# Kernel tuning notes

Measured on AMD Instinct MI355X. Metric: run time of the kernel, lower is better.

Reference implementation:

```python
import jax, jax.numpy as jnp
import numpy as np

NUM_HEADS = 16
EMBED_DIM = 1024
HEAD_DIM = EMBED_DIM // NUM_HEADS  # 64


def setup_inputs() -> dict:
    key = jax.random.key(0)
    k1, k2, k3 = jax.random.split(key, 3)
    x = jax.random.normal(k1, (2, 2048, EMBED_DIM), dtype=jnp.float32)
    # torch Linear(head_dim, 3*head_dim): weight [3*hd, hd], bias [3*hd]
    # stored here as W_qkv [hd, 3*hd] so that y = x @ W_qkv + b
    lim = 1.0 / np.sqrt(HEAD_DIM)
    W_qkv = jax.random.uniform(k2, (HEAD_DIM, 3 * HEAD_DIM), minval=-lim, maxval=lim, dtype=jnp.float32)
    b_qkv = jax.random.uniform(k3, (3 * HEAD_DIM,), minval=-lim, maxval=lim, dtype=jnp.float32)
    return {"x": x, "W_qkv": W_qkv, "b_qkv": b_qkv}


def reference(x, W_qkv, b_qkv):
    B, T, E = x.shape
    # [B, T, E] -> [B, H, T, hd]
    xh = x.reshape(B, T, NUM_HEADS, HEAD_DIM).transpose(0, 2, 1, 3)
    qkv = xh @ W_qkv + b_qkv  # [B, H, T, 3*hd], shared weights across heads
    q, k, v = jnp.split(qkv, 3, axis=-1)
    scale = 1.0 / jnp.sqrt(jnp.asarray(HEAD_DIM, dtype=x.dtype))
    scores = jnp.einsum('bhqd,bhkd->bhqk', q, k) * scale  # [B, H, T, T]
    attn = jax.nn.softmax(scores, axis=-1)
    out = jnp.einsum('bhqk,bhkd->bhqd', attn, v)  # [B, H, T, hd]
    return out.transpose(0, 2, 1, 3).reshape(B, T, E)
```

## Files before the change

### kernel.cpp

```cpp
#include <hip/hip_runtime.h>
#include <hip/hip_bf16.h>

#define T_SEQ   2048
#define EMBED   1024
#define HD      64
#define NHEADS  16
#define NBH     32
#define QSCALE  0.18033688011112042f

typedef __attribute__((ext_vector_type(8))) short short8;
typedef __attribute__((ext_vector_type(4))) float f32x4;
typedef __attribute__((ext_vector_type(2))) unsigned int uint2v;

#if __has_builtin(__builtin_amdgcn_exp2f)
#define EXP2F __builtin_amdgcn_exp2f
#else
#define EXP2F exp2f
#endif

__device__ __forceinline__ ushort bf16r(float f) {
  union { float f; unsigned u; } v; v.f = f;
  return (ushort)((v.u + 0x8000u) >> 16);
}

__device__ __forceinline__ unsigned pk2bf_perm(float a, float b) {
  union { float f; unsigned u; } ua, ub; ua.f = a; ub.f = b;
  return __builtin_amdgcn_perm(ub.u + 0x8000u, ua.u + 0x8000u, 0x07060302u);
}
#if __has_builtin(__builtin_amdgcn_cvt_pk_bf16_f32)
typedef __attribute__((ext_vector_type(2))) __bf16 bf16x2;
__device__ __forceinline__ unsigned pkbf(float a, float b) {
  union { bf16x2 v; unsigned u; } c;
  c.v = __builtin_amdgcn_cvt_pk_bf16_f32(a, b);
  return c.u;
}
#else
#define pkbf pk2bf_perm
#endif

__device__ __forceinline__ void async16(const ushort* g, ushort* l) {
  __builtin_amdgcn_global_load_lds(
      (const __attribute__((address_space(1))) unsigned int*)g,
      (__attribute__((address_space(3))) unsigned int*)l, 16, 0, 0);
}

__global__ __launch_bounds__(256) void prep_w(const float* __restrict__ W,
                                              ushort* __restrict__ Wg) {
  const int i = blockIdx.x * 256 + threadIdx.x;
  const int d = i / 192, c = i - d * 192;
  const int phys = c * 64 + (((d >> 3) ^ (c & 7)) << 3) + (d & 7);
  Wg[phys] = bf16r(W[i]);
}

__global__ __launch_bounds__(256) void qkv_proj(
    const float* __restrict__ x, const ushort* __restrict__ Wg,
    const float* __restrict__ bias,
    ushort* __restrict__ Qws, ushort* __restrict__ Kws,
    ushort* __restrict__ Vtws) {
  __shared__ ushort WtL[192 * 64];
  __shared__ float bl[192];

  const int bx = blockIdx.x;
  const int b  = bx >> 9;
  const int h  = (bx >> 5) & 15;
  const int t0 = (bx & 31) * 64;
  const int tid = threadIdx.x;
  const int wave = tid >> 6, lane = tid & 63;
  const int quad = lane >> 4, n16 = lane & 15;

  const int trow = t0 + wave * 16 + n16;
  const float* xr = x + ((size_t)(b * T_SEQ + trow)) * EMBED + h * HD;
  short8 xa[2];
#pragma unroll
  for (int ks = 0; ks < 2; ks++) {
    f32x4 v0 = *(const f32x4*)(xr + ks * 32 + quad * 8);
    f32x4 v1 = *(const f32x4*)(xr + ks * 32 + quad * 8 + 4);
    short8 f;
    ((unsigned*)&f)[0] = pkbf(v0[0], v0[1]);
    ((unsigned*)&f)[1] = pkbf(v0[2], v0[3]);
    ((unsigned*)&f)[2] = pkbf(v1[0], v1[1]);
    ((unsigned*)&f)[3] = pkbf(v1[2], v1[3]);
    xa[ks] = f;
  }

#pragma unroll
  for (int it = 0; it < 6; it++)
    async16(Wg + it * 2048 + tid * 8, WtL + it * 2048 + wave * 512);
  if (tid < 192) bl[tid] = bias[tid];
  __syncthreads();

  const int bh = b * NHEADS + h;
  const size_t qkbase = (size_t)bh * T_SEQ * HD;
  const int tw = t0 + wave * 16;
  const int sw = n16 & 7;

#pragma unroll
  for (int nt = 0; nt < 12; nt++) {
    const ushort* wrow = WtL + (nt * 16 + n16) * 64;
    const short8 wb0 = *(short8*)(wrow + ((quad ^ sw) << 3));
    const short8 wb1 = *(short8*)(wrow + (((4 | quad) ^ sw) << 3));
    const float bv = bl[nt * 16 + n16];
    f32x4 acc = (f32x4){0.f, 0.f, 0.f, 0.f};
    acc = __builtin_amdgcn_mfma_f32_16x16x32_bf16(xa[0], wb0, acc, 0, 0, 0);
    acc = __builtin_amdgcn_mfma_f32_16x16x32_bf16(xa[1], wb1, acc, 0, 0, 0);
    if (nt < 4) {
      const int d = nt * 16 + n16;
#pragma unroll
      for (int r = 0; r < 4; r++)
        Qws[qkbase + (size_t)(tw + quad * 4 + r) * HD + d] =
            bf16r((acc[r] + bv) * QSCALE);
    } else if (nt < 8) {
      const int d = (nt - 4) * 16 + n16;
#pragma unroll
      for (int r = 0; r < 4; r++)
        Kws[qkbase + (size_t)(tw + quad * 4 + r) * HD + d] =
            bf16r(acc[r] + bv);
    } else {
      const int d = (nt - 8) * 16 + n16;
      const int tcol = tw + quad * 4;
      uint2v pk;
      pk.x = pkbf(acc[0] + bv, acc[1] + bv);
      pk.y = pkbf(acc[2] + bv, acc[3] + bv);
      *(uint2v*)(Vtws + (size_t)(bh * HD + d) * T_SEQ + tcol) = pk;
    }
  }
}

__global__ __launch_bounds__(256) void flash_attn(
    const ushort* __restrict__ Qws, const ushort* __restrict__ Kws,
    const ushort* __restrict__ Vtws, float* __restrict__ out) {
  __shared__ ushort Ks[2][64 * 64];
  __shared__ ushort Vs[2][64 * 64];
  __shared__ ushort Ps[4 * 16 * 64];

  const int bx = blockIdx.x;
  const int bh = bx & 31;
  const int q0 = (bx >> 5) * 64;
  const int b = bh >> 4, h = bh & 15;
  const int tid = threadIdx.x;
  const int wave = tid >> 6, lane = tid & 63;
  const int quad = lane >> 4, n16 = lane & 15;

  const ushort* Qb = Qws + (size_t)bh * T_SEQ * HD;
  const ushort* Kb = Kws + (size_t)bh * T_SEQ * HD;
  const ushort* Vb = Vtws + (size_t)bh * HD * T_SEQ;

  short8 qa[2];
#pragma unroll
  for (int ks = 0; ks < 2; ks++) {
    const int row = q0 + wave * 16 + n16;
    qa[ks] = *(const short8*)(Qb + (size_t)row * HD + ks * 32 + quad * 8);
  }

  const int sr = tid >> 3, sp = tid & 7;
  const int sl = (sp ^ (sr & 7)) * 8;
  const ushort* srcK0 = Kb + (size_t)sr * HD + sl;
  const ushort* srcK1 = Kb + (size_t)(sr + 32) * HD + sl;
  const ushort* srcV0 = Vb + (size_t)sr * T_SEQ + sl;
  const ushort* srcV1 = Vb + (size_t)(sr + 32) * T_SEQ + sl;

  int foff[2];
#pragma unroll
  for (int ks = 0; ks < 2; ks++)
    foff[ks] = n16 * 64 + ((((ks << 2) | quad) ^ (n16 & 7)) << 3);

  f32x4 o[4];
  float lsum = 0.f;
#pragma unroll
  for (int nt = 0; nt < 4; nt++) o[nt] = (f32x4){0.f, 0.f, 0.f, 0.f};

  ushort* Pw = Ps + wave * 1024;

  async16(srcK0, Ks[0] + wave * 512);
  async16(srcK1, Ks[0] + 2048 + wave * 512);
  async16(srcV0, Vs[0] + wave * 512);
  async16(srcV1, Vs[0] + 2048 + wave * 512);
  __syncthreads();

  for (int kt = 0; kt < 32; kt++) {
    const int bsel = kt & 1;
    if (kt < 31) {
      const size_t kK = (size_t)(kt + 1) * 64 * HD;
      const size_t kV = (size_t)(kt + 1) * 64;
      async16(srcK0 + kK, Ks[bsel ^ 1] + wave * 512);
      async16(srcK1 + kK, Ks[bsel ^ 1] + 2048 + wave * 512);
      async16(srcV0 + kV, Vs[bsel ^ 1] + wave * 512);
      async16(srcV1 + kV, Vs[bsel ^ 1] + 2048 + wave * 512);
    }
    const ushort* Kt = Ks[bsel];
    const ushort* Vt = Vs[bsel];

    f32x4 s[4];
#pragma unroll
    for (int nt = 0; nt < 4; nt++) {
      const short8 ka0 = *(short8*)(Kt + (nt << 10) + foff[0]);
      const short8 ka1 = *(short8*)(Kt + (nt << 10) + foff[1]);
      f32x4 acc = (f32x4){0.f, 0.f, 0.f, 0.f};
      acc = __builtin_amdgcn_mfma_f32_16x16x32_bf16(ka0, qa[0], acc, 0, 0, 0);
      acc = __builtin_amdgcn_mfma_f32_16x16x32_bf16(ka1, qa[1], acc, 0, 0, 0);
      s[nt] = acc;
    }

#pragma unroll
    for (int nt = 0; nt < 4; nt++) {
      float p0 = EXP2F(s[nt][0]), p1 = EXP2F(s[nt][1]);
      float p2 = EXP2F(s[nt][2]), p3 = EXP2F(s[nt][3]);
      lsum += (p0 + p1) + (p2 + p3);
      uint2v pk;
      pk.x = pkbf(p0, p1);
      pk.y = pkbf(p2, p3);
      *(uint2v*)(Pw + n16 * 64 +
                 ((((nt << 1) | (quad >> 1)) ^ (n16 & 7)) << 3) +
                 ((quad & 1) << 2)) = pk;
    }

    short8 pa0 = *(short8*)(Pw + foff[0]);
    short8 pa1 = *(short8*)(Pw + foff[1]);
#pragma unroll
    for (int nt = 0; nt < 4; nt++) {
      const short8 vb0 = *(short8*)(Vt + (nt << 10) + foff[0]);
      const short8 vb1 = *(short8*)(Vt + (nt << 10) + foff[1]);
      o[nt] = __builtin_amdgcn_mfma_f32_16x16x32_bf16(pa0, vb0, o[nt], 0, 0, 0);
      o[nt] = __builtin_amdgcn_mfma_f32_16x16x32_bf16(pa1, vb1, o[nt], 0, 0, 0);
    }
    __syncthreads();
  }

  lsum += __shfl_xor(lsum, 16, 64);
  lsum += __shfl_xor(lsum, 32, 64);
  float* Lw = (float*)Pw;
  if (lane < 16) Lw[n16] = lsum;

#pragma unroll
  for (int r = 0; r < 4; r++) {
    const int row = q0 + wave * 16 + quad * 4 + r;
    const float rl = 1.0f / Lw[quad * 4 + r];
#pragma unroll
    for (int nt = 0; nt < 4; nt++) {
      const int d = nt * 16 + n16;
      out[(size_t)(b * T_SEQ + row) * EMBED + h * HD + d] = o[nt][r] * rl;
    }
  }
}

extern "C" void kernel_launch(void* const* d_in, const int* in_sizes, int n_in,
                              void* d_out, int out_size, void* d_ws, size_t ws_size,
                              hipStream_t stream) {
  (void)in_sizes; (void)n_in; (void)out_size; (void)ws_size;
  const float* x    = (const float*)d_in[0];
  const float* W    = (const float*)d_in[1];
  const float* bias = (const float*)d_in[2];
  float* out = (float*)d_out;

  const size_t elems = (size_t)NBH * T_SEQ * HD;
  ushort* Qws  = (ushort*)d_ws;
  ushort* Kws  = Qws + elems;
  ushort* Vtws = Kws + elems;
  ushort* Wg   = Vtws + elems;

  prep_w<<<dim3(48), dim3(256), 0, stream>>>(W, Wg);
  qkv_proj<<<dim3(1024), dim3(256), 0, stream>>>(x, Wg, bias, Qws, Kws, Vtws);
  flash_attn<<<dim3(1024), dim3(256), 0, stream>>>(Qws, Kws, Vtws, out);
}
```

Baseline: 135.9 us.

## Double query rows per wave and move P transpose into registers via permlane swaps

Each block now handles 128 query rows instead of 64, with each wave computing two 16-row halves. Every K/V tile loaded into LDS therefore feeds twice as many MFMAs, and the grid shrinks to 512 blocks. The P matrix is no longer written to and re-read from shared memory. It is rearranged into the MFMA A-operand layout with permlane32/permlane16 swap instructions, and the final row sums are broadcast by shuffle. The cost is more registers per thread and fewer blocks, which may lower occupancy and leave some CUs with less work.

```diff
diff --git a/kernel.cpp b/kernel.cpp
--- a/kernel.cpp
+++ b/kernel.cpp
@@ -11,6 +11,7 @@
 typedef __attribute__((ext_vector_type(8))) short short8;
 typedef __attribute__((ext_vector_type(4))) float f32x4;
 typedef __attribute__((ext_vector_type(2))) unsigned int uint2v;
+typedef __attribute__((ext_vector_type(4))) unsigned int uint4v;
 
 #if __has_builtin(__builtin_amdgcn_exp2f)
 #define EXP2F __builtin_amdgcn_exp2f
@@ -37,6 +38,23 @@
 #else
 #define pkbf pk2bf_perm
 #endif
+
+__device__ __forceinline__ uint2v pl32swap(unsigned a, unsigned b) {
+#if __has_builtin(__builtin_amdgcn_permlane32_swap)
+  return __builtin_amdgcn_permlane32_swap(a, b, false, false);
+#else
+  asm("v_permlane32_swap_b32 %0, %1" : "+v"(a), "+v"(b));
+  return (uint2v){a, b};
+#endif
+}
+__device__ __forceinline__ uint2v pl16swap(unsigned a, unsigned b) {
+#if __has_builtin(__builtin_amdgcn_permlane16_swap)
+  return __builtin_amdgcn_permlane16_swap(a, b, false, false);
+#else
+  asm("v_permlane16_swap_b32 %0, %1" : "+v"(a), "+v"(b));
+  return (uint2v){a, b};
+#endif
+}
 
 __device__ __forceinline__ void async16(const ushort* g, ushort* l) {
   __builtin_amdgcn_global_load_lds(
@@ -131,11 +149,10 @@
     const ushort* __restrict__ Vtws, float* __restrict__ out) {
   __shared__ ushort Ks[2][64 * 64];
   __shared__ ushort Vs[2][64 * 64];
-  __shared__ ushort Ps[4 * 16 * 64];
 
   const int bx = blockIdx.x;
   const int bh = bx & 31;
-  const int q0 = (bx >> 5) * 64;
+  const int q0 = (bx >> 5) * 128;
   const int b = bh >> 4, h = bh & 15;
   const int tid = threadIdx.x;
   const int wave = tid >> 6, lane = tid & 63;
@@ -145,12 +162,14 @@
   const ushort* Kb = Kws + (size_t)bh * T_SEQ * HD;
   const ushort* Vb = Vtws + (size_t)bh * HD * T_SEQ;
 
-  short8 qa[2];
-#pragma unroll
-  for (int ks = 0; ks < 2; ks++) {
-    const int row = q0 + wave * 16 + n16;
-    qa[ks] = *(const short8*)(Qb + (size_t)row * HD + ks * 32 + quad * 8);
-  }
+  short8 qa[2][2];
+#pragma unroll
+  for (int hf = 0; hf < 2; hf++)
+#pragma unroll
+    for (int ks = 0; ks < 2; ks++) {
+      const int row = q0 + wave * 32 + hf * 16 + n16;
+      qa[hf][ks] = *(const short8*)(Qb + (size_t)row * HD + ks * 32 + quad * 8);
+    }
 
   const int sr = tid >> 3, sp = tid & 7;
   const int sl = (sp ^ (sr & 7)) * 8;
@@ -164,12 +183,12 @@
   for (int ks = 0; ks < 2; ks++)
     foff[ks] = n16 * 64 + ((((ks << 2) | quad) ^ (n16 & 7)) << 3);
 
-  f32x4 o[4];
-  float lsum = 0.f;
-#pragma unroll
-  for (int nt = 0; nt < 4; nt++) o[nt] = (f32x4){0.f, 0.f, 0.f, 0.f};
-
-  ushort* Pw = Ps + wave * 1024;
+  f32x4 o[2][4];
+  float ls[2] = {0.f, 0.f};
+#pragma unroll
+  for (int hf = 0; hf < 2; hf++)
+#pragma unroll
+    for (int nt = 0; nt < 4; nt++) o[hf][nt] = (f32x4){0.f, 0.f, 0.f, 0.f};
 
   async16(srcK0, Ks[0] + wave * 512);
   async16(srcK1, Ks[0] + 2048 + wave * 512);
@@ -190,55 +209,77 @@
     const ushort* Kt = Ks[bsel];
     const ushort* Vt = Vs[bsel];
 
-    f32x4 s[4];
+    f32x4 s0[4], s1[4];
 #pragma unroll
     for (int nt = 0; nt < 4; nt++) {
       const short8 ka0 = *(short8*)(Kt + (nt << 10) + foff[0]);
       const short8 ka1 = *(short8*)(Kt + (nt << 10) + foff[1]);
-      f32x4 acc = (f32x4){0.f, 0.f, 0.f, 0.f};
-      acc = __builtin_amdgcn_mfma_f32_16x16x32_bf16(ka0, qa[0], acc, 0, 0, 0);
-      acc = __builtin_amdgcn_mfma_f32_16x16x32_bf16(ka1, qa[1], acc, 0, 0, 0);
-      s[nt] = acc;
-    }
-
-#pragma unroll
-    for (int nt = 0; nt < 4; nt++) {
-      float p0 = EXP2F(s[nt][0]), p1 = EXP2F(s[nt][1]);
-      float p2 = EXP2F(s[nt][2]), p3 = EXP2F(s[nt][3]);
-      lsum += (p0 + p1) + (p2 + p3);
-      uint2v pk;
-      pk.x = pkbf(p0, p1);
-      pk.y = pkbf(p2, p3);
-      *(uint2v*)(Pw + n16 * 64 +
-                 ((((nt << 1) | (quad >> 1)) ^ (n16 & 7)) << 3) +
-                 ((quad & 1) << 2)) = pk;
-    }
-
-    short8 pa0 = *(short8*)(Pw + foff[0]);
-    short8 pa1 = *(short8*)(Pw + foff[1]);
+      f32x4 a0 = (f32x4){0.f, 0.f, 0.f, 0.f};
+      f32x4 a1 = (f32x4){0.f, 0.f, 0.f, 0.f};
+      a0 = __builtin_amdgcn_mfma_f32_16x16x32_bf16(ka0, qa[0][0], a0, 0, 0, 0);
+      a0 = __builtin_amdgcn_mfma_f32_16x16x32_bf16(ka1, qa[0][1], a0, 0, 0, 0);
+      a1 = __builtin_amdgcn_mfma_f32_16x16x32_bf16(ka0, qa[1][0], a1, 0, 0, 0);
+      a1 = __builtin_amdgcn_mfma_f32_16x16x32_bf16(ka1, qa[1][1], a1, 0, 0, 0);
+      s0[nt] = a0;
+      s1[nt] = a1;
+    }
+
+    short8 pa[2][2];
+#pragma unroll
+    for (int hf = 0; hf < 2; hf++) {
+      unsigned P01[4], P23[4];
+      float lacc = 0.f;
+#pragma unroll
+      for (int nt = 0; nt < 4; nt++) {
+        const f32x4 sv = hf ? s1[nt] : s0[nt];
+        float p0 = EXP2F(sv[0]), p1 = EXP2F(sv[1]);
+        float p2 = EXP2F(sv[2]), p3 = EXP2F(sv[3]);
+        lacc += (p0 + p1) + (p2 + p3);
+        P01[nt] = pkbf(p0, p1);
+        P23[nt] = pkbf(p2, p3);
+      }
+      ls[hf] += lacc;
+#pragma unroll
+      for (int ks = 0; ks < 2; ks++) {
+        uint2v tA = pl32swap(P01[2 * ks], P01[2 * ks + 1]);
+        uint2v uA = pl16swap(tA.x, tA.y);
+        uint2v tB = pl32swap(P23[2 * ks], P23[2 * ks + 1]);
+        uint2v uB = pl16swap(tB.x, tB.y);
+        union { uint4v u; short8 s; } c;
+        c.u = (uint4v){uA.x, uB.x, uA.y, uB.y};
+        pa[hf][ks] = c.s;
+      }
+    }
+
 #pragma unroll
     for (int nt = 0; nt < 4; nt++) {
       const short8 vb0 = *(short8*)(Vt + (nt << 10) + foff[0]);
       const short8 vb1 = *(short8*)(Vt + (nt << 10) + foff[1]);
-      o[nt] = __builtin_amdgcn_mfma_f32_16x16x32_bf16(pa0, vb0, o[nt], 0, 0, 0);
-      o[nt] = __builtin_amdgcn_mfma_f32_16x16x32_bf16(pa1, vb1, o[nt], 0, 0, 0);
+      o[0][nt] = __builtin_amdgcn_mfma_f32_16x16x32_bf16(pa[0][0], vb0, o[0][nt], 0, 0, 0);
+      o[0][nt] = __builtin_amdgcn_mfma_f32_16x16x32_bf16(pa[0][1], vb1, o[0][nt], 0, 0, 0);
+      o[1][nt] = __builtin_amdgcn_mfma_f32_16x16x32_bf16(pa[1][0], vb0, o[1][nt], 0, 0, 0);
+      o[1][nt] = __builtin_amdgcn_mfma_f32_16x16x32_bf16(pa[1][1], vb1, o[1][nt], 0, 0, 0);
     }
     __syncthreads();
   }
 
-  lsum += __shfl_xor(lsum, 16, 64);
-  lsum += __shfl_xor(lsum, 32, 64);
-  float* Lw = (float*)Pw;
-  if (lane < 16) Lw[n16] = lsum;
-
-#pragma unroll
-  for (int r = 0; r < 4; r++) {
-    const int row = q0 + wave * 16 + quad * 4 + r;
-    const float rl = 1.0f / Lw[quad * 4 + r];
-#pragma unroll
-    for (int nt = 0; nt < 4; nt++) {
-      const int d = nt * 16 + n16;
-      out[(size_t)(b * T_SEQ + row) * EMBED + h * HD + d] = o[nt][r] * rl;
+#pragma unroll
+  for (int hf = 0; hf < 2; hf++) {
+    ls[hf] += __shfl_xor(ls[hf], 16, 64);
+    ls[hf] += __shfl_xor(ls[hf], 32, 64);
+  }
+
+#pragma unroll
+  for (int hf = 0; hf < 2; hf++) {
+#pragma unroll
+    for (int r = 0; r < 4; r++) {
+      const float rl = 1.0f / __shfl(ls[hf], quad * 4 + r, 64);
+      const int row = q0 + wave * 32 + hf * 16 + quad * 4 + r;
+#pragma unroll
+      for (int nt = 0; nt < 4; nt++) {
+        const int d = nt * 16 + n16;
+        out[(size_t)(b * T_SEQ + row) * EMBED + h * HD + d] = o[hf][nt][r] * rl;
+      }
     }
   }
 }
@@ -260,5 +301,5 @@
 
   prep_w<<<dim3(48), dim3(256), 0, stream>>>(W, Wg);
   qkv_proj<<<dim3(1024), dim3(256), 0, stream>>>(x, Wg, bias, Qws, Kws, Vtws);
-  flash_attn<<<dim3(1024), dim3(256), 0, stream>>>(Qws, Kws, Vtws, out);
-}
+  flash_attn<<<dim3(512), dim3(256), 0, stream>>>(Qws, Kws, Vtws, out);
+}
```

After: 133.7 us. Within noise of the previous version (-1.7%).
